# Kernel tuning notes

Measured on AMD Instinct MI355X. Metric: run time of the kernel, lower is better.

Reference implementation:

```python
import jax, jax.numpy as jnp
import numpy as np

UP = (2, 2)  # up_size


def setup_inputs() -> dict:
    key = jax.random.key(0)
    k1, k2, k3 = jax.random.split(key, 3)
    B, H, W, C = 16, 64, 64, 256
    H2, W2 = H * UP[0], W * UP[1]
    updates = jax.random.normal(k1, (B, H, W, C), dtype=jnp.float32)
    # Build a consistent argmax mask: each pooled cell points at a random
    # position within its up_size window of the unpooled output.
    dy = jax.random.randint(k2, (B, H, W, C), 0, UP[0])
    dx = jax.random.randint(k3, (B, H, W, C), 0, UP[1])
    b = jnp.arange(B)[:, None, None, None]
    y = jnp.arange(H)[None, :, None, None] * UP[0] + dy
    x = jnp.arange(W)[None, None, :, None] * UP[1] + dx
    f = jnp.arange(C)[None, None, None, :]
    mask = ((b * H2 + y) * W2 + x) * C + f  # flat index into [B,H2,W2,C]
    return {"updates": updates, "mask": mask.astype(jnp.int32)}


def reference(updates, mask):
    B, H, W, C = updates.shape
    H2, W2 = H * UP[0], W * UP[1]
    mask = mask.astype(jnp.int32)
    one = jnp.ones_like(mask)
    b = one * jnp.arange(B, dtype=jnp.int32)[:, None, None, None]
    f = one * jnp.arange(C, dtype=jnp.int32)[None, None, None, :]
    # Recover spatial coords from flat mask (same arithmetic as the TF code)
    y = (mask - f) // (W2 * C) - b * H2
    x = (mask // C) % W2
    # scatter_nd semantics: zeros base, duplicate indices accumulate
    out = jnp.zeros((B, H2, W2, C), dtype=updates.dtype)
    out = out.at[b, y, x, f].add(updates)
    return out
```

## Files before the change

### kernel.cpp

```cpp
#include <hip/hip_runtime.h>


typedef float  f32x4 __attribute__((ext_vector_type(4)));
typedef int    i32x4 __attribute__((ext_vector_type(4)));

constexpr int B = 16, H = 64, W = 64, C = 256;
constexpr int W2 = 128;
constexpr int TOTAL4 = B * H * W * C / 4;

__global__ __launch_bounds__(256) void
unpool_gather_kernel(const f32x4* __restrict__ upd,
                     const i32x4* __restrict__ msk,
                     f32x4* __restrict__ out)
{
    int i = blockIdx.x * blockDim.x + threadIdx.x;

    int c  = (i & 63) << 2;
    int sp = i >> 6;
    int w  = sp & 63;
    int hb = sp >> 6;

    int o00 = 2 * (hb * W2 + w) * C + c;
    int o01 = o00 + C;
    int o10 = o00 + W2 * C;
    int o11 = o10 + C;

    i32x4 m = __builtin_nontemporal_load(msk + i);
    f32x4 u = __builtin_nontemporal_load(upd + i);

    f32x4 r00, r01, r10, r11;
    #pragma unroll
    for (int j = 0; j < 4; ++j) {
        r00[j] = (m[j] == o00 + j) ? u[j] : 0.0f;
        r01[j] = (m[j] == o01 + j) ? u[j] : 0.0f;
        r10[j] = (m[j] == o10 + j) ? u[j] : 0.0f;
        r11[j] = (m[j] == o11 + j) ? u[j] : 0.0f;
    }

    __builtin_nontemporal_store(r00, out + (o00 >> 2));
    __builtin_nontemporal_store(r01, out + (o01 >> 2));
    __builtin_nontemporal_store(r10, out + (o10 >> 2));
    __builtin_nontemporal_store(r11, out + (o11 >> 2));
}

extern "C" void kernel_launch(void* const* d_in, const int* in_sizes, int n_in,
                              void* d_out, int out_size, void* d_ws, size_t ws_size,
                              hipStream_t stream)
{
    const f32x4* upd = (const f32x4*)d_in[0];
    const i32x4* msk = (const i32x4*)d_in[1];
    f32x4*       out = (f32x4*)d_out;

    constexpr int BLK = 256;
    constexpr int GRID = TOTAL4 / BLK;
    unpool_gather_kernel<<<GRID, BLK, 0, stream>>>(upd, msk, out);
}
```

Measured before the change: 74.42 us.

## Map one thread per output vector instead of per input vector

The kernel now assigns each thread one float4 of the output and reads the matching input and mask entries, instead of each thread reading one input vector and writing four output vectors. Output stores become fully contiguous per wavefront. Each input element is now loaded by four threads, relying on cache hits, and the input loads are no longer nontemporal. The grid is four times larger.

```diff
diff --git a/kernel.cpp b/kernel.cpp
--- a/kernel.cpp
+++ b/kernel.cpp
@@ -5,42 +5,34 @@
 typedef int    i32x4 __attribute__((ext_vector_type(4)));
 
 constexpr int B = 16, H = 64, W = 64, C = 256;
-constexpr int W2 = 128;
-constexpr int TOTAL4 = B * H * W * C / 4;
+constexpr int OUT4 = B * (2*H) * (2*W) * C / 4;
+constexpr int BLK  = 256;
+constexpr int GRID = OUT4 / BLK;
 
 __global__ __launch_bounds__(256) void
-unpool_gather_kernel(const f32x4* __restrict__ upd,
-                     const i32x4* __restrict__ msk,
-                     f32x4* __restrict__ out)
+unpool_gather_out_kernel(const f32x4* __restrict__ upd,
+                         const i32x4* __restrict__ msk,
+                         f32x4* __restrict__ out)
 {
-    int i = blockIdx.x * blockDim.x + threadIdx.x;
+    int tid = blockIdx.x * blockDim.x + threadIdx.x;
 
-    int c  = (i & 63) << 2;
-    int sp = i >> 6;
-    int w  = sp & 63;
-    int hb = sp >> 6;
+    int cq = tid & 63;
+    int x  = (tid >> 6)  & 127;
+    int y  = (tid >> 13) & 127;
+    int b  =  tid >> 20;
 
-    int o00 = 2 * (hb * W2 + w) * C + c;
-    int o01 = o00 + C;
-    int o10 = o00 + W2 * C;
-    int o11 = o10 + C;
+    int iin = (b << 18) | ((y >> 1) << 12) | ((x >> 1) << 6) | cq;
 
-    i32x4 m = __builtin_nontemporal_load(msk + i);
-    f32x4 u = __builtin_nontemporal_load(upd + i);
+    i32x4 m = msk[iin];
+    f32x4 u = upd[iin];
 
-    f32x4 r00, r01, r10, r11;
+    int o = tid << 2;
+    f32x4 r;
     #pragma unroll
-    for (int j = 0; j < 4; ++j) {
-        r00[j] = (m[j] == o00 + j) ? u[j] : 0.0f;
-        r01[j] = (m[j] == o01 + j) ? u[j] : 0.0f;
-        r10[j] = (m[j] == o10 + j) ? u[j] : 0.0f;
-        r11[j] = (m[j] == o11 + j) ? u[j] : 0.0f;
-    }
+    for (int j = 0; j < 4; ++j)
+        r[j] = (m[j] == o + j) ? u[j] : 0.0f;
 
-    __builtin_nontemporal_store(r00, out + (o00 >> 2));
-    __builtin_nontemporal_store(r01, out + (o01 >> 2));
-    __builtin_nontemporal_store(r10, out + (o10 >> 2));
-    __builtin_nontemporal_store(r11, out + (o11 >> 2));
+    __builtin_nontemporal_store(r, out + tid);
 }
 
 extern "C" void kernel_launch(void* const* d_in, const int* in_sizes, int n_in,
@@ -51,7 +43,5 @@
     const i32x4* msk = (const i32x4*)d_in[1];
     f32x4*       out = (f32x4*)d_out;
 
-    constexpr int BLK = 256;
-    constexpr int GRID = TOTAL4 / BLK;
-    unpool_gather_kernel<<<GRID, BLK, 0, stream>>>(upd, msk, out);
+    unpool_gather_out_kernel<<<GRID, BLK, 0, stream>>>(upd, msk, out);
 }
```

New measurement: 60.45 us. 1.23x faster.
